# Performance work log

Hardware: AMD Instinct MI355X
Metric: run time of the kernel (lower is better)

## Reference

```python
import jax, jax.numpy as jnp
import numpy as np

N_NODES = 100000


def _gcn_conv(h, src, dst, norm, W, b, n):
    # linear transform then symmetric-normalized scatter-add aggregation
    hw = h @ W                                   # [N, out]
    msg = hw[src] * norm[:, None]                # [E+N, out] gathered messages
    out = jax.ops.segment_sum(msg, dst, num_segments=n)
    return out + b


def _self_loops_and_norm(edge_index, n):
    loop = jnp.arange(n, dtype=edge_index.dtype)
    src = jnp.concatenate([edge_index[0], loop])
    dst = jnp.concatenate([edge_index[1], loop])
    deg = jax.ops.segment_sum(jnp.ones_like(src, dtype=jnp.float32), dst, num_segments=n)
    dinv = jnp.where(deg > 0, jax.lax.rsqrt(jnp.maximum(deg, 1.0)), 0.0)
    norm = dinv[src] * dinv[dst]                 # D^-1/2 (A+I) D^-1/2 coefficients
    return src, dst, norm


def setup_inputs() -> dict:
    key = jax.random.key(0)
    k1, k2, k3, k4 = jax.random.split(key, 4)
    F_IN, H, C = 128, 64, 40
    x = jax.random.normal(k1, (N_NODES, F_IN), dtype=jnp.float32)
    edge_index = jax.random.randint(k2, (2, 3200000), 0, N_NODES, dtype=jnp.int64)
    s1 = 1.0 / np.sqrt(F_IN)
    s2 = 1.0 / np.sqrt(H)
    W1 = jax.random.uniform(k3, (F_IN, H), jnp.float32, -s1, s1)
    b1 = jnp.zeros((H,), jnp.float32)
    W2 = jax.random.uniform(k4, (H, C), jnp.float32, -s2, s2)
    b2 = jnp.zeros((C,), jnp.float32)
    return {"x": x, "edge_index": edge_index, "W1": W1, "b1": b1, "W2": W2, "b2": b2}


def reference(x, edge_index, W1, b1, W2, b2):
    n = x.shape[0]
    src, dst, norm = _self_loops_and_norm(edge_index, n)
    h = _gcn_conv(x, src, dst, norm, W1, b1, n)
    h = jax.nn.relu(h)
    # dropout(p=0.5) is identity in eval mode
    out = _gcn_conv(h, src, dst, norm, W2, b2, n)
    return jax.nn.log_softmax(out, axis=1)
```

## Files before the change

kernel.cpp:

```cpp
#include <hip/hip_runtime.h>
#include <math.h>

#define F_IN 128
#define HID  64
#define NCLS 40
#define PART_CHUNK 4096
#define CAP 4608
#define CAPX 768
#define MAXNB 1024
#define ASTRIDE 132

typedef _Float16 half8 __attribute__((ext_vector_type(8)));
typedef _Float16 half2t __attribute__((ext_vector_type(2)));
typedef float floatx4 __attribute__((ext_vector_type(4)));

__device__ inline half8 ld_half8_u8(const _Float16* p) {
    union { uint2 u[2]; half8 h; } r;
    r.u[0] = *(const uint2*)p;
    r.u[1] = *(const uint2*)(p + 4);
    return r.h;
}

__global__ __launch_bounds__(256) void fused_part_gemm1(const int* __restrict__ src,
                                                        const int* __restrict__ dst,
                                                        int* __restrict__ bCur,
                                                        int* __restrict__ pkBuf,
                                                        int E, int NB, int nPart,
                                                        const float* __restrict__ x,
                                                        const float* __restrict__ W1,
                                                        _Float16* __restrict__ h1, int n) {
    __shared__ __align__(16) char smem[2 * 64 * ASTRIDE * 2];
    int tid = threadIdx.x;
    if ((int)blockIdx.x < nPart) {
        int xcd = (int)blockIdx.x & 7;
        int* hcnt  = (int*)smem;
        int* hbase = (int*)smem + MAXNB;
        for (int i = tid; i < NB; i += 256) hcnt[i] = 0;
        __syncthreads();
        int e0 = blockIdx.x * PART_CHUNK;
        int s_[16], d_[16];
#pragma unroll
        for (int i = 0; i < 16; ++i) {
            int e = e0 + i * 256 + tid;
            if (e < E) {
                s_[i] = src[e]; d_[i] = dst[e];
                atomicAdd(&hcnt[d_[i] >> 7], 1);
            }
        }
        __syncthreads();
        for (int b = tid; b < NB; b += 256) {
            int c = hcnt[b];
            hbase[b] = c ? ((b * 8 + xcd) * CAPX + atomicAdd(&bCur[b * 8 + xcd], c)) : 0;
            hcnt[b] = 0;
        }
        __syncthreads();
#pragma unroll
        for (int i = 0; i < 16; ++i) {
            int e = e0 + i * 256 + tid;
            if (e < E) {
                int b = d_[i] >> 7;
                int loc = atomicAdd(&hcnt[b], 1);
                pkBuf[hbase[b] + loc] = (s_[i] << 7) | (d_[i] & 127);
            }
        }
    } else {
        _Float16* Ah = (_Float16*)smem;
        _Float16* Wt = Ah + 64 * ASTRIDE;
        int node0 = ((int)blockIdx.x - nPart) * 64;
#pragma unroll
        for (int i = 0; i < 8; ++i) {
            int f = (i * 256 + tid) * 4;
            int m = f >> 7, k = f & 127;
            float4 v = (node0 + m < n) ? ((const float4*)(x + (size_t)(node0 + m) * F_IN))[k >> 2]
                                       : make_float4(0.f, 0.f, 0.f, 0.f);
            _Float16* p = &Ah[m * ASTRIDE + k];
            p[0] = (_Float16)v.x; p[1] = (_Float16)v.y; p[2] = (_Float16)v.z; p[3] = (_Float16)v.w;
        }
#pragma unroll
        for (int i = 0; i < 32; ++i) {
            int f = i * 256 + tid;
            int k = f >> 6, nn = f & 63;
            Wt[nn * ASTRIDE + k] = (_Float16)W1[f];
        }
        __syncthreads();
        int wave = tid >> 6, lane = tid & 63;
        int m0 = wave * 16;
        int col = lane & 15, quad = lane >> 4;
        floatx4 acc[4] = {{0,0,0,0},{0,0,0,0},{0,0,0,0},{0,0,0,0}};
#pragma unroll
        for (int kk = 0; kk < 4; ++kk) {
            int kbase = kk * 32 + quad * 8;
            half8 a = ld_half8_u8(&Ah[(m0 + col) * ASTRIDE + kbase]);
#pragma unroll
            for (int t = 0; t < 4; ++t) {
                half8 b = ld_half8_u8(&Wt[(t * 16 + col) * ASTRIDE + kbase]);
                acc[t] = __builtin_amdgcn_mfma_f32_16x16x32_f16(a, b, acc[t], 0, 0, 0);
            }
        }
#pragma unroll
        for (int t = 0; t < 4; ++t)
#pragma unroll
            for (int r = 0; r < 4; ++r) {
                int node = node0 + m0 + quad * 4 + r;
                if (node < n) h1[(size_t)node * HID + t * 16 + col] = (_Float16)acc[t][r];
            }
    }
}

__global__ __launch_bounds__(256) void scan_buckets(const int* __restrict__ bCur,
                                                    int* __restrict__ bBase, int NB, int E) {
    __shared__ int part[256];
    int tid = threadIdx.x;
    int v[4]; int sum = 0;
#pragma unroll
    for (int k = 0; k < 4; ++k) {
        int i = tid * 4 + k;
        int s = 0;
        if (i < NB) {
#pragma unroll
            for (int x = 0; x < 8; ++x) s += bCur[i * 8 + x];
        }
        v[k] = s;
        sum += s;
    }
    part[tid] = sum; __syncthreads();
    for (int off = 1; off < 256; off <<= 1) {
        int t = (tid >= off) ? part[tid - off] : 0;
        __syncthreads();
        part[tid] += t;
        __syncthreads();
    }
    int base = part[tid] - sum;
#pragma unroll
    for (int k = 0; k < 4; ++k) {
        int i = tid * 4 + k;
        if (i < NB) bBase[i] = base;
        base += v[k];
    }
    if (tid == 255) bBase[NB] = E;
}

__global__ __launch_bounds__(256) void bucket_finalize(const int* __restrict__ bCur,
                                                       const int* __restrict__ bBase,
                                                       const int* __restrict__ pkBuf,
                                                       int* __restrict__ ptr,
                                                       float* __restrict__ dinv,
                                                       int* __restrict__ sIdx, int n, int E) {
    __shared__ int cnt128[128];
    __shared__ int sc[128];
    __shared__ int cur[128];
    __shared__ int segoff[9];
    __shared__ int ebuf[CAP];
    __shared__ int stage[CAP];
    int b = blockIdx.x;
    int node0 = b << 7;
    int tid = threadIdx.x;
    if (tid < 128) cnt128[tid] = 0;
    if (tid == 0) {
        int o = 0;
#pragma unroll
        for (int x = 0; x < 8; ++x) { segoff[x] = o; o += bCur[b * 8 + x]; }
        segoff[8] = o;
    }
    __syncthreads();
    int cnt = segoff[8];
    int dbase = bBase[b];
    for (int x = 0; x < 8; ++x) {
        int off = segoff[x], len = segoff[x + 1] - off;
        const int* s = pkBuf + (size_t)(b * 8 + x) * CAPX;
        for (int j = tid; j < len; j += 256) {
            int p = s[j];
            ebuf[off + j] = p;
            atomicAdd(&cnt128[p & 127], 1);
        }
    }
    __syncthreads();
    int v = (tid < 128) ? cnt128[tid] : 0;
    if (tid < 128) sc[tid] = v;
    __syncthreads();
    for (int off = 1; off < 128; off <<= 1) {
        int t = (tid < 128 && tid >= off) ? sc[tid - off] : 0;
        __syncthreads();
        if (tid < 128) sc[tid] += t;
        __syncthreads();
    }
    if (tid < 128) {
        cur[tid] = sc[tid] - v;
        int node = node0 + tid;
        if (node < n) {
            ptr[node] = dbase + sc[tid] - v;
            dinv[node] = rsqrtf((float)v + 1.0f);
        }
    }
    if (tid == 0 && b == gridDim.x - 1) ptr[n] = E;
    __syncthreads();
    for (int j = tid; j < cnt; j += 256) {
        int p = ebuf[j];
        int pos = atomicAdd(&cur[p & 127], 1);
        stage[pos] = p >> 7;
    }
    __syncthreads();
    for (int j = tid; j < cnt; j += 256)
        sIdx[dbase + j] = stage[j];
}

template<bool RELU>
__global__ __launch_bounds__(256) void gather4(const int* __restrict__ ptr,
                                               const int* __restrict__ sIdx,
                                               const float* __restrict__ dinv,
                                               const _Float16* __restrict__ hin,
                                               const float* __restrict__ bias,
                                               _Float16* __restrict__ hout, int n) {
    int tid = threadIdx.x, wave = tid >> 6, lane = tid & 63;
    int ng   = lane >> 4;
    int slot = (lane >> 3) & 1;
    int fq   = lane & 7;
    int node = blockIdx.x * 16 + wave * 4 + ng;
    bool valid = node < n;
    int nodeC = valid ? node : 0;
    int beg = ptr[nodeC];
    int end = valid ? ptr[nodeC + 1] : beg;
    float di = dinv[nodeC];
    float a0[8] = {0,0,0,0,0,0,0,0}, a1[8] = {0,0,0,0,0,0,0,0};

    if (slot == 0 && valid) {
        half8 v = *(const half8*)(hin + nodeC * HID + fq * 8);
        float w = di * di;
#pragma unroll
        for (int j = 0; j < 8; ++j) a0[j] = (float)v[j] * w;
    }
    for (int j0 = beg; j0 < end; j0 += 8) {
        int ja = j0 + slot, jb = j0 + 2 + slot, jc = j0 + 4 + slot, jd = j0 + 6 + slot;
        bool va = ja < end, vb = jb < end, vc = jc < end, vd = jd < end;
        int sa = sIdx[va ? ja : beg];
        int sb = sIdx[vb ? jb : beg];
        int sc_ = sIdx[vc ? jc : beg];
        int sd = sIdx[vd ? jd : beg];
        float wa = va ? dinv[sa] * di : 0.f;
        float wb = vb ? dinv[sb] * di : 0.f;
        float wc = vc ? dinv[sc_] * di : 0.f;
        float wd = vd ? dinv[sd] * di : 0.f;
        half8 ra = *(const half8*)(hin + sa * HID + fq * 8);
        half8 rb = *(const half8*)(hin + sb * HID + fq * 8);
        half8 rc = *(const half8*)(hin + sc_ * HID + fq * 8);
        half8 rd = *(const half8*)(hin + sd * HID + fq * 8);
#if __has_builtin(__builtin_amdgcn_fdot2)
        half2t wab = { (_Float16)wa, (_Float16)wb };
        half2t wcd = { (_Float16)wc, (_Float16)wd };
#pragma unroll
        for (int j = 0; j < 8; ++j) {
            half2t pab = { ra[j], rb[j] };
            half2t pcd = { rc[j], rd[j] };
            a0[j] = __builtin_amdgcn_fdot2(pab, wab, a0[j], false);
            a1[j] = __builtin_amdgcn_fdot2(pcd, wcd, a1[j], false);
        }
#else
#pragma unroll
        for (int j = 0; j < 8; ++j) {
            a0[j] = fmaf((float)ra[j], wa, a0[j]);
            a0[j] = fmaf((float)rb[j], wb, a0[j]);
            a1[j] = fmaf((float)rc[j], wc, a1[j]);
            a1[j] = fmaf((float)rd[j], wd, a1[j]);
        }
#endif
    }
#pragma unroll
    for (int j = 0; j < 8; ++j) {
        a0[j] += a1[j];
        a0[j] += __shfl_xor(a0[j], 8, 64);
    }
    if (slot == 0 && valid) {
        union { half8 h; uint4 u; } o;
#pragma unroll
        for (int j = 0; j < 8; ++j) {
            float v = a0[j];
            if (RELU) v = fmaxf(v + bias[fq * 8 + j], 0.f);
            o.h[j] = (_Float16)v;
        }
        *(uint4*)(hout + nodeC * HID + fq * 8) = o.u;
    }
}

#define GSTRIDE 72
__global__ __launch_bounds__(256) void gemm2_mfma_logsm(const _Float16* __restrict__ g,
                                                        const float* __restrict__ W2,
                                                        const float* __restrict__ b2,
                                                        float* __restrict__ out, int n) {
    __shared__ _Float16 gt[64 * GSTRIDE];
    __shared__ _Float16 wt[48 * GSTRIDE];
    int tid = threadIdx.x;
    int node0 = blockIdx.x * 64;
#pragma unroll
    for (int i = 0; i < 2; ++i) {
        int f = (i * 256 + tid) * 8;
        int m = f >> 6, k = f & 63;
        union { uint4 u; half8 h; } v;
        if (node0 + m < n) v.u = *(const uint4*)(g + (size_t)(node0 + m) * HID + k);
        else v.u = make_uint4(0, 0, 0, 0);
        *(uint4*)&gt[m * GSTRIDE + k] = v.u;
    }
#pragma unroll
    for (int i = 0; i < 12; ++i) {
        int f = i * 256 + tid;
        int c = f >> 6, k = f & 63;
        wt[c * GSTRIDE + k] = (c < NCLS) ? (_Float16)W2[k * NCLS + c] : (_Float16)0.f;
    }
    __syncthreads();

    int wave = tid >> 6, lane = tid & 63;
    int m0 = wave * 16;
    int col = lane & 15, quad = lane >> 4;
    floatx4 acc[3] = {{0,0,0,0},{0,0,0,0},{0,0,0,0}};
#pragma unroll
    for (int kk = 0; kk < 2; ++kk) {
        int kbase = kk * 32 + quad * 8;
        half8 a = *(const half8*)&gt[(m0 + col) * GSTRIDE + kbase];
#pragma unroll
        for (int t = 0; t < 3; ++t) {
            half8 b = *(const half8*)&wt[(t * 16 + col) * GSTRIDE + kbase];
            acc[t] = __builtin_amdgcn_mfma_f32_16x16x32_f16(a, b, acc[t], 0, 0, 0);
        }
    }
    float bb[3];
#pragma unroll
    for (int t = 0; t < 3; ++t) {
        int c = t * 16 + col;
        bb[t] = (c < NCLS) ? b2[c] : 0.f;
    }
#pragma unroll
    for (int r = 0; r < 4; ++r) {
        int node = node0 + m0 + quad * 4 + r;
        float v0 = acc[0][r] + bb[0];
        float v1 = acc[1][r] + bb[1];
        float v2 = (col < 8) ? acc[2][r] + bb[2] : -INFINITY;
        float m = fmaxf(fmaxf(v0, v1), v2);
#pragma unroll
        for (int off = 1; off < 16; off <<= 1) m = fmaxf(m, __shfl_xor(m, off, 64));
        float s = expf(v0 - m) + expf(v1 - m) + ((col < 8) ? expf(v2 - m) : 0.f);
#pragma unroll
        for (int off = 1; off < 16; off <<= 1) s += __shfl_xor(s, off, 64);
        float ls = logf(s);
        if (node < n) {
            float* op = out + (size_t)node * NCLS;
            op[col]      = v0 - m - ls;
            op[16 + col] = v1 - m - ls;
            if (col < 8) op[32 + col] = v2 - m - ls;
        }
    }
}

extern "C" void kernel_launch(void* const* d_in, const int* in_sizes, int n_in,
                              void* d_out, int out_size, void* d_ws, size_t ws_size,
                              hipStream_t stream) {
    const float* x  = (const float*)d_in[0];
    const int*   ei = (const int*)d_in[1];
    const float* W1 = (const float*)d_in[2];
    const float* b1 = (const float*)d_in[3];
    const float* W2 = (const float*)d_in[4];
    const float* b2 = (const float*)d_in[5];
    float* out = (float*)d_out;

    int n = in_sizes[0] / F_IN;
    int E = in_sizes[1] / 2;
    const int* src = ei;
    const int* dst = ei + E;
    int NB = (n + 127) >> 7;
    int nPart = (E + PART_CHUNK - 1) / PART_CHUNK;
    int nGemm1 = (n + 63) / 64;

    char* ws = (char*)d_ws;
    const size_t MB = 1024 * 1024;
    int*      bCur  = (int*)  (ws);
    int*      bBase = (int*)  (ws + 64 * 1024);
    int*      ptr   = (int*)  (ws + 128 * 1024);
    float*    dinv  = (float*)(ws + 1 * MB);
    int*      sIdx  = (int*)     (ws + 2 * MB);
    _Float16* bufA  = (_Float16*)(ws + 15 * MB);
    int*      pkBuf = (int*)     (ws + 28 * MB);
    _Float16* bufB  = (_Float16*)(ws + 28 * MB);

    hipMemsetAsync(bCur, 0, (size_t)NB * 8 * sizeof(int), stream);
    fused_part_gemm1<<<nPart + nGemm1, 256, 0, stream>>>(src, dst, bCur, pkBuf, E, NB, nPart,
                                                         x, W1, bufA, n);
    scan_buckets<<<1, 256, 0, stream>>>(bCur, bBase, NB, E);
    bucket_finalize<<<NB, 256, 0, stream>>>(bCur, bBase, pkBuf, ptr, dinv, sIdx, n, E);

    gather4<true ><<<(n + 15) / 16, 256, 0, stream>>>(ptr, sIdx, dinv, bufA, b1, bufB, n);
    gather4<false><<<(n + 15) / 16, 256, 0, stream>>>(ptr, sIdx, dinv, bufB, b1, bufA, n);
    gemm2_mfma_logsm<<<(n + 63) / 64, 256, 0, stream>>>(bufA, W2, b2, out, n);
}
```

Before: 320.9 us.

## Prescale node features by dinv to remove per-edge dinv gathers in aggregation

```diff
diff --git a/kernel.cpp b/kernel.cpp
--- a/kernel.cpp
+++ b/kernel.cpp
@@ -145,10 +145,13 @@
                                                        const int* __restrict__ pkBuf,
                                                        int* __restrict__ ptr,
                                                        float* __restrict__ dinv,
-                                                       int* __restrict__ sIdx, int n, int E) {
+                                                       int* __restrict__ sIdx,
+                                                       _Float16* __restrict__ h1,
+                                                       int n, int E) {
     __shared__ int cnt128[128];
     __shared__ int sc[128];
     __shared__ int cur[128];
+    __shared__ float sdinv[128];
     __shared__ int segoff[9];
     __shared__ int ebuf[CAP];
     __shared__ int stage[CAP];
@@ -186,10 +189,12 @@
     }
     if (tid < 128) {
         cur[tid] = sc[tid] - v;
+        float dv = rsqrtf((float)v + 1.0f);
+        sdinv[tid] = dv;
         int node = node0 + tid;
         if (node < n) {
             ptr[node] = dbase + sc[tid] - v;
-            dinv[node] = rsqrtf((float)v + 1.0f);
+            dinv[node] = dv;
         }
     }
     if (tid == 0 && b == gridDim.x - 1) ptr[n] = E;
@@ -202,6 +207,19 @@
     __syncthreads();
     for (int j = tid; j < cnt; j += 256)
         sIdx[dbase + j] = stage[j];
+#pragma unroll
+    for (int pass = 0; pass < 4; ++pass) {
+        int idx = pass * 256 + tid;
+        int nd = node0 + (idx >> 3);
+        if (nd < n) {
+            float dv = sdinv[idx >> 3];
+            half8* p = (half8*)(h1 + (size_t)nd * HID) + (idx & 7);
+            half8 hv = *p;
+#pragma unroll
+            for (int j = 0; j < 8; ++j) hv[j] = (_Float16)((float)hv[j] * dv);
+            *p = hv;
+        }
+    }
 }
 
 template<bool RELU>
@@ -225,10 +243,10 @@
 
     if (slot == 0 && valid) {
         half8 v = *(const half8*)(hin + nodeC * HID + fq * 8);
-        float w = di * di;
-#pragma unroll
-        for (int j = 0; j < 8; ++j) a0[j] = (float)v[j] * w;
-    }
+#pragma unroll
+        for (int j = 0; j < 8; ++j) a0[j] = (float)v[j];
+    }
+    const _Float16 ONE = (_Float16)1.0f, ZEROH = (_Float16)0.0f;
     for (int j0 = beg; j0 < end; j0 += 8) {
         int ja = j0 + slot, jb = j0 + 2 + slot, jc = j0 + 4 + slot, jd = j0 + 6 + slot;
         bool va = ja < end, vb = jb < end, vc = jc < end, vd = jd < end;
@@ -236,17 +254,13 @@
         int sb = sIdx[vb ? jb : beg];
         int sc_ = sIdx[vc ? jc : beg];
         int sd = sIdx[vd ? jd : beg];
-        float wa = va ? dinv[sa] * di : 0.f;
-        float wb = vb ? dinv[sb] * di : 0.f;
-        float wc = vc ? dinv[sc_] * di : 0.f;
-        float wd = vd ? dinv[sd] * di : 0.f;
         half8 ra = *(const half8*)(hin + sa * HID + fq * 8);
         half8 rb = *(const half8*)(hin + sb * HID + fq * 8);
         half8 rc = *(const half8*)(hin + sc_ * HID + fq * 8);
         half8 rd = *(const half8*)(hin + sd * HID + fq * 8);
 #if __has_builtin(__builtin_amdgcn_fdot2)
-        half2t wab = { (_Float16)wa, (_Float16)wb };
-        half2t wcd = { (_Float16)wc, (_Float16)wd };
+        half2t wab = { va ? ONE : ZEROH, vb ? ONE : ZEROH };
+        half2t wcd = { vc ? ONE : ZEROH, vd ? ONE : ZEROH };
 #pragma unroll
         for (int j = 0; j < 8; ++j) {
             half2t pab = { ra[j], rb[j] };
@@ -255,6 +269,7 @@
             a1[j] = __builtin_amdgcn_fdot2(pcd, wcd, a1[j], false);
         }
 #else
+        float wa = va ? 1.f : 0.f, wb = vb ? 1.f : 0.f, wc = vc ? 1.f : 0.f, wd = vd ? 1.f : 0.f;
 #pragma unroll
         for (int j = 0; j < 8; ++j) {
             a0[j] = fmaf((float)ra[j], wa, a0[j]);
@@ -273,8 +288,8 @@
         union { half8 h; uint4 u; } o;
 #pragma unroll
         for (int j = 0; j < 8; ++j) {
-            float v = a0[j];
-            if (RELU) v = fmaxf(v + bias[fq * 8 + j], 0.f);
+            float v = di * a0[j];
+            if (RELU) v = fmaxf(v + bias[fq * 8 + j], 0.f) * di;
             o.h[j] = (_Float16)v;
         }
         *(uint4*)(hout + nodeC * HID + fq * 8) = o.u;
@@ -383,7 +398,7 @@
     fused_part_gemm1<<<nPart + nGemm1, 256, 0, stream>>>(src, dst, bCur, pkBuf, E, NB, nPart,
                                                          x, W1, bufA, n);
     scan_buckets<<<1, 256, 0, stream>>>(bCur, bBase, NB, E);
-    bucket_finalize<<<NB, 256, 0, stream>>>(bCur, bBase, pkBuf, ptr, dinv, sIdx, n, E);
+    bucket_finalize<<<NB, 256, 0, stream>>>(bCur, bBase, pkBuf, ptr, dinv, sIdx, bufA, n, E);
 
     gather4<true ><<<(n + 15) / 16, 256, 0, stream>>>(ptr, sIdx, dinv, bufA, b1, bufB, n);
     gather4<false><<<(n + 15) / 16, 256, 0, stream>>>(ptr, sIdx, dinv, bufB, b1, bufA, n);
```

Result: faster. 299.6 us (-6.6%).
